# Kernel optimization log

Hardware: AMD Instinct MI355X
Metric: run time of the kernel (lower is better)

The kernel has to match this reference:

```python
import jax, jax.numpy as jnp
import numpy as np

HEADS = 8
BLOCK = 32

def setup_inputs() -> dict:
    key = jax.random.key(0)
    ks = jax.random.split(key, 4)
    b, n, d, f = 4, 4096, 1024, 128
    x = jax.random.normal(ks[0], (b, n, d), dtype=jnp.float32)
    w_qkv = jax.random.normal(ks[1], (3 * d, d), dtype=jnp.float32) * (d ** -0.5)
    w_out = jax.random.normal(ks[2], (d, d), dtype=jnp.float32) * (d ** -0.5)
    b_out = jnp.zeros((d,), dtype=jnp.float32)
    proj = jax.random.normal(ks[3], (HEADS, d // HEADS, f), dtype=jnp.float32) * ((d // HEADS) ** -0.5)
    return {"x": x, "w_qkv": w_qkv, "w_out": w_out, "b_out": b_out, "proj": proj}

def reference(x, w_qkv, w_out, b_out, proj):
    b, n, d = x.shape
    h = HEADS
    hd = d // h
    nb = n // BLOCK
    # QKV projection (torch Linear: x @ W.T)
    qkv = x @ w_qkv.T  # (b, n, 3d)
    q, k, v = jnp.split(qkv, 3, axis=-1)
    def to_blocks(t):
        # (b, n, d) -> (b, h, nb, BLOCK, hd)
        return t.reshape(b, n, h, hd).transpose(0, 2, 1, 3).reshape(b, h, nb, BLOCK, hd)
    q, k, v = to_blocks(q), to_blocks(k), to_blocks(v)
    # per-head feature map: elu(x @ proj) + 1
    qp = jax.nn.elu(jnp.einsum('bhcsd,hdf->bhcsf', q, proj)) + 1.0
    kp = jax.nn.elu(jnp.einsum('bhcsd,hdf->bhcsf', k, proj)) + 1.0
    # per-block kv state and normalizer
    kv = jnp.einsum('bhcsf,bhcsd->bhcfd', kp, v)          # (b,h,nb,f,hd)
    num = jnp.einsum('bhcsf,bhcfd->bhcsd', qp, kv)        # (b,h,nb,BLOCK,hd)
    ksum = kp.sum(axis=3)                                 # (b,h,nb,f)
    z = 1.0 / (jnp.einsum('bhcsf,bhcf->bhcs', qp, ksum) + 1e-8)
    out = num * z[..., None]
    # merge blocks and heads: (b,h,nb,BLOCK,hd) -> (b,n,d)
    out = out.reshape(b, h, n, hd).transpose(0, 2, 1, 3).reshape(b, n, d)
    # output projection (dropout inert in eval)
    return out @ w_out.T + b_out
```

## Files before the change

kernel.cpp:

```cpp
#include <hip/hip_runtime.h>
#include <hip/hip_bf16.h>
#include <stdint.h>
#include <stddef.h>

typedef __bf16 bf16_t;
typedef __bf16 bf16x8 __attribute__((ext_vector_type(8)));
typedef __bf16 bf16x4 __attribute__((ext_vector_type(4)));
typedef float  f32x4  __attribute__((ext_vector_type(4)));

static __device__ __forceinline__ f32x4 mfma16x16x32(bf16x8 a, bf16x8 b, f32x4 c) {
  return __builtin_amdgcn_mfma_f32_16x16x32_bf16(a, b, c, 0, 0, 0);
}

static __device__ __forceinline__ void gld_lds16(const void* g, void* l) {
  __builtin_amdgcn_global_load_lds(
      (const __attribute__((address_space(1))) unsigned int*)g,
      (__attribute__((address_space(3))) unsigned int*)l, 16, 0, 0);
}

#define BARW()   __builtin_amdgcn_s_barrier()
#define SCHED0() __builtin_amdgcn_sched_barrier(0)
#define LGKM0()  asm volatile("s_waitcnt lgkmcnt(0)" ::: "memory")
#define VMCNT(n) asm volatile("s_waitcnt vmcnt(" #n ")" ::: "memory")
#define PRIO(p)  __builtin_amdgcn_s_setprio(p)

__global__ __launch_bounds__(256) void prep(const float* __restrict__ wqkv,
                                            const float* __restrict__ proj,
                                            const float* __restrict__ wout,
                                            const float* __restrict__ x,
                                            bf16_t* __restrict__ B1t2,
                                            bf16_t* __restrict__ Wv,
                                            bf16_t* __restrict__ W3t,
                                            bf16_t* __restrict__ xbf) {
  const int b = blockIdx.x;
  const int tid = threadIdx.x;
  if (b >= 768) {
    for (int i = (b - 768) * 256 + tid; i < 4194304; i += 262144) {
      float4 v = *(const float4*)(x + (size_t)i * 4);
      bf16x4 o;
      o[0] = (bf16_t)v.x; o[1] = (bf16_t)v.y; o[2] = (bf16_t)v.z; o[3] = (bf16_t)v.w;
      *(bf16x4*)(xbf + (size_t)i * 4) = o;
    }
    return;
  }
  if (b >= 256) {
    const float* src = (b < 512) ? wout : (wqkv + (size_t)2048 * 1024);
    bf16_t* dst = (b < 512) ? W3t : Wv;
    size_t off = ((size_t)((b & 255)) * 4096) + tid * 16;
#pragma unroll
    for (int it = 0; it < 4; ++it) {
      float4 v = *(const float4*)(src + off + it * 4);
      bf16x4 o;
      o[0] = (bf16_t)v.x; o[1] = (bf16_t)v.y; o[2] = (bf16_t)v.z; o[3] = (bf16_t)v.w;
      *(bf16x4*)(dst + off + it * 4) = o;
    }
    return;
  }
  const int combo  = b >> 4;
  const int kt     = b & 15;
  const int qk     = combo >> 3;
  const int h      = combo & 7;
  const int klocal = tid & 63;
  const int fg     = tid >> 6;
  const int k      = kt * 64 + klocal;

  const float* wbase = wqkv + ((size_t)(qk * 1024 + h * 128)) * 1024 + k;
  const float* pbase = proj + (size_t)h * 16384 + fg * 32;

  float acc[32];
#pragma unroll
  for (int i = 0; i < 32; ++i) acc[i] = 0.f;

  for (int c = 0; c < 128; ++c) {
    float a = wbase[(size_t)c * 1024];
    const float4* p = (const float4*)(pbase + (size_t)c * 128);
#pragma unroll
    for (int i = 0; i < 8; ++i) {
      float4 pv = p[i];
      acc[i * 4 + 0] += a * pv.x;
      acc[i * 4 + 1] += a * pv.y;
      acc[i * 4 + 2] += a * pv.z;
      acc[i * 4 + 3] += a * pv.w;
    }
  }
  bf16_t* obase = B1t2 + ((size_t)(h * 256 + qk * 128 + fg * 32)) * 1024 + k;
#pragma unroll
  for (int i = 0; i < 32; ++i) obase[(size_t)i * 1024] = (bf16_t)acc[i];
}

#define GEMM_MAINLOOP_DECLS()                                                  \
  const int tid  = threadIdx.x;                                                \
  const int lane = tid & 63;                                                   \
  const int wid  = tid >> 6;                                                   \
  const int wm   = wid >> 2;                                                   \
  const int wn   = wid & 3;                                                    \
  const int lr   = lane & 15;                                                  \
  const int g0   = lane >> 4;                                                  \
  int srow[2], sgl[2];                                                         \
  _Pragma("unroll")                                                            \
  for (int l = 0; l < 2; ++l) {                                                \
    int idx = l * 512 + tid;                                                   \
    srow[l] = idx >> 3;                                                        \
    sgl[l]  = (idx & 7) ^ (srow[l] & 7);                                       \
  }

#define STAGE_T(arr, base, half, kt, K_)                                       \
  {                                                                            \
    const bf16_t* s_ = (base) + (size_t)((half) * 128) * (K_) + (kt) * 64;     \
    bf16_t* d_ = &(arr)[half][0];                                              \
    _Pragma("unroll")                                                          \
    for (int l_ = 0; l_ < 2; ++l_)                                             \
      gld_lds16(s_ + (size_t)srow[l_] * (K_) + sgl[l_] * 8,                    \
                d_ + (l_ * 512 + tid) * 8);                                    \
  }

#define RD_A(buf, qm)                                                          \
  _Pragma("unroll")                                                            \
  for (int t_ = 0; t_ < 4; ++t_) {                                             \
    int r_ = (qm) * 64 + t_ * 16 + lr;                                         \
    _Pragma("unroll")                                                          \
    for (int kh_ = 0; kh_ < 2; ++kh_) {                                        \
      int gl_ = (g0 + kh_ * 4) ^ (r_ & 7);                                     \
      a[t_][kh_] = *(const bf16x8*)(&sA[buf][wm][r_ * 64 + gl_ * 8]);          \
    }                                                                          \
  }
#define RD_B(buf, qn, breg)                                                    \
  _Pragma("unroll")                                                            \
  for (int u_ = 0; u_ < 2; ++u_) {                                             \
    int r_ = (wn & 1) * 64 + (qn) * 32 + u_ * 16 + lr;                         \
    _Pragma("unroll")                                                          \
    for (int kh_ = 0; kh_ < 2; ++kh_) {                                        \
      int gl_ = (g0 + kh_ * 4) ^ (r_ & 7);                                     \
      breg[u_][kh_] = *(const bf16x8*)(&sB[buf][wn >> 1][r_ * 64 + gl_ * 8]);  \
    }                                                                          \
  }
#define MMA(qm, qn, breg)                                                      \
  _Pragma("unroll")                                                            \
  for (int mi_ = 0; mi_ < 4; ++mi_)                                            \
    _Pragma("unroll")                                                          \
    for (int nj_ = 0; nj_ < 2; ++nj_)                                          \
      _Pragma("unroll")                                                        \
      for (int kh_ = 0; kh_ < 2; ++kh_)                                        \
        acc[(qm) * 4 + mi_][(qn) * 2 + nj_] =                                  \
            mfma16x16x32(a[mi_][kh_], breg[nj_][kh_],                          \
                         acc[(qm) * 4 + mi_][(qn) * 2 + nj_]);

#define GEMM_MAINLOOP_BODY(Abase, Bbase, K_, NT_)                              \
  f32x4 acc[8][4] = {};                                                        \
  bf16x8 a[4][2], b0[2][2], b1[2][2];                                          \
  STAGE_T(sB[0], Bbase, 0, 0, K_); STAGE_T(sA[0], Abase, 0, 0, K_);            \
  STAGE_T(sB[0], Bbase, 1, 0, K_); STAGE_T(sA[0], Abase, 1, 0, K_);            \
  STAGE_T(sB[1], Bbase, 0, 1, K_); STAGE_T(sA[1], Abase, 0, 1, K_);            \
  VMCNT(4);                                                                    \
  BARW();                                                                      \
  _Pragma("unroll 2")                                                          \
  for (int j = 0; j < (NT_); ++j) {                                            \
    const int cur = j & 1;                                                     \
    const int nxt = cur ^ 1;                                                   \
                       \
    RD_A(cur, 0);                                                              \
    RD_B(cur, 0, b0);                                                          \
    if (j + 1 < (NT_)) { STAGE_T(sB[nxt], Bbase, 1, j + 1, K_); }              \
    SCHED0(); BARW(); LGKM0(); SCHED0();                                       \
    PRIO(1); MMA(0, 0, b0); PRIO(0);                                           \
    SCHED0(); BARW();                                                          \
                             \
    RD_B(cur, 1, b1);                                                          \
    if (j + 1 < (NT_)) { STAGE_T(sA[nxt], Abase, 1, j + 1, K_); }              \
    SCHED0(); BARW(); LGKM0(); SCHED0();                                       \
    PRIO(1); MMA(0, 1, b1); PRIO(0);                                           \
    SCHED0(); BARW();                                                          \
                             \
    RD_A(cur, 1);                                                              \
    if (j + 2 < (NT_)) { STAGE_T(sB[cur], Bbase, 0, j + 2, K_); }              \
    SCHED0(); BARW(); LGKM0(); SCHED0();                                       \
    PRIO(1); MMA(1, 1, b1); PRIO(0);                                           \
    SCHED0(); BARW();                                                          \
                           \
    if (j + 2 < (NT_)) { STAGE_T(sA[cur], Abase, 0, j + 2, K_); }              \
    SCHED0(); BARW();                                                          \
    PRIO(1); MMA(1, 0, b0); PRIO(0);                                           \
    if (j + 2 < (NT_)) { VMCNT(4); } else { VMCNT(0); }                        \
    SCHED0(); BARW();                                                          \
  }

template <int EPI>
__global__ __launch_bounds__(512, 2) void gemm256(const bf16_t* __restrict__ A,
                                                  const bf16_t* __restrict__ Bt,
                                                  void* __restrict__ Cout,
                                                  const float* __restrict__ bias,
                                                  int N, int K, int NB) {
  __shared__ __align__(16) bf16_t sA[2][2][8192];
  __shared__ __align__(16) bf16_t sB[2][2][8192];
  GEMM_MAINLOOP_DECLS();

  const int nwg = gridDim.x;
  const int cpx = nwg >> 3;
  const int bid = blockIdx.x;
  const int swz = (bid & 7) * cpx + (bid >> 3);
  const int m0 = (swz / NB) * 256;
  const int n0 = (swz % NB) * 256;
  const int NT = K >> 6;

  const bf16_t* Abase = A  + (size_t)m0 * K;
  const bf16_t* Bbase = Bt + (size_t)n0 * K;

  GEMM_MAINLOOP_BODY(Abase, Bbase, K, NT);

#pragma unroll
  for (int i = 0; i < 8; ++i) {
#pragma unroll
    for (int jn = 0; jn < 4; ++jn) {
      const int n = n0 + wn * 64 + jn * 16 + lr;
#pragma unroll
      for (int r = 0; r < 4; ++r) {
        const int m = m0 + wm * 128 + i * 16 + g0 * 4 + r;
        float v = acc[i][jn][r];
        if constexpr (EPI == 2) {
          ((float*)Cout)[(size_t)m * N + n] = v + bias[n];
        } else {
          ((bf16_t*)Cout)[(size_t)m * N + n] = (bf16_t)v;
        }
      }
    }
  }
}

__global__ __launch_bounds__(512, 2) void gemm_fused(const bf16_t* __restrict__ A,
                                                     const bf16_t* __restrict__ Bt,
                                                     const bf16_t* __restrict__ VtG,
                                                     bf16_t* __restrict__ OUT1) {
  __shared__ __align__(16) bf16_t sA[2][2][8192];
  __shared__ __align__(16) bf16_t sB[2][2][8192];
  GEMM_MAINLOOP_DECLS();

  const int nwg = gridDim.x;
  const int cpx = nwg >> 3;
  const int bid = blockIdx.x;
  const int swz = (bid & 7) * cpx + (bid >> 3);
  const int m0 = (swz >> 3) * 256;
  const int h  = swz & 7;
  const int K  = 1024;
  const int NT = 16;

  const bf16_t* Abase = A  + (size_t)m0 * K;
  const bf16_t* Bbase = Bt + (size_t)(h * 256) * K;

  GEMM_MAINLOOP_BODY(Abase, Bbase, K, NT);

  char* sQb = (char*)(&sA[0][0][0]);
  char* sKb = (char*)(&sB[0][0][0]);

  {
    char* dbase = (wn < 2) ? sQb : sKb;
#pragma unroll
    for (int i = 0; i < 8; ++i)
#pragma unroll
      for (int jn = 0; jn < 4; ++jn)
#pragma unroll
        for (int r = 0; r < 4; ++r) {
          int row = wm * 128 + i * 16 + g0 * 4 + r;
          int col = (wn & 1) * 64 + jn * 16 + lr;
          float v = acc[i][jn][r];
          v = v > 0.f ? v + 1.f : __expf(v);
          int gq = col >> 3;
          int g  = (gq & 8) | ((gq ^ row) & 7);
          *(bf16_t*)(dbase + row * 256 + g * 16 + (col & 7) * 2) = (bf16_t)v;
        }
  }
  LGKM0();
  BARW();

  const int cb = wm * 4 + wn;
  const int rb = cb * 32;
  bf16x8 aS[4][2], bS[4][2];
#pragma unroll
  for (int kh = 0; kh < 4; ++kh) {
#pragma unroll
    for (int t = 0; t < 2; ++t) {
      int row = rb + t * 16 + lr;
      int gq = kh * 4 + g0;
      int g  = (gq & 8) | ((gq ^ row) & 7);
      aS[kh][t] = *(const bf16x8*)(sQb + row * 256 + g * 16);
      bS[kh][t] = *(const bf16x8*)(sKb + row * 256 + g * 16);
    }
  }
  SCHED0(); LGKM0(); BARW();

  {
#pragma unroll
    for (int l = 0; l < 8; ++l) {
      int gd = l * 512 + tid;
      int row = gd >> 5, gcol = gd & 31;
      const bf16_t* src = VtG + (size_t)(h * 128 + row) * 16384 + m0 +
                          ((gcol ^ (row & 7)) * 8);
      gld_lds16(src, sKb + gd * 16);
    }
  }
  SCHED0();

  f32x4 sacc[2][2] = {};
#pragma unroll
  for (int kh = 0; kh < 4; ++kh)
#pragma unroll
    for (int mt = 0; mt < 2; ++mt)
#pragma unroll
      for (int nt = 0; nt < 2; ++nt)
        sacc[mt][nt] = mfma16x16x32(aS[kh][mt], bS[kh][nt], sacc[mt][nt]);

  float zin[2][4];
#pragma unroll
  for (int mt = 0; mt < 2; ++mt)
#pragma unroll
    for (int r = 0; r < 4; ++r) {
      float s = sacc[mt][0][r] + sacc[mt][1][r];
      s += __shfl_xor(s, 1); s += __shfl_xor(s, 2);
      s += __shfl_xor(s, 4); s += __shfl_xor(s, 8);
      zin[mt][r] = 1.0f / (s + 1e-8f);
    }

  char* Pl = sQb;
#pragma unroll
  for (int mt = 0; mt < 2; ++mt)
#pragma unroll
    for (int nt = 0; nt < 2; ++nt)
#pragma unroll
      for (int r = 0; r < 4; ++r) {
        int i = mt * 16 + g0 * 4 + r;
        int jj = nt * 16 + lr;
        *(bf16_t*)(Pl + cb * 2560 + i * 80 + jj * 2) =
            (bf16_t)(sacc[mt][nt][r] * zin[mt][r]);
      }
  LGKM0();
  VMCNT(0);
  BARW();

  bf16x8 aP[2];
#pragma unroll
  for (int mt = 0; mt < 2; ++mt)
    aP[mt] = *(const bf16x8*)(Pl + cb * 2560 + (mt * 16 + lr) * 80 + g0 * 16);
#pragma unroll
  for (int dt = 0; dt < 8; ++dt) {
    int row = dt * 16 + lr;
    int gidx = cb * 4 + g0;
    int g = (gidx & 24) | ((gidx ^ row) & 7);
    bf16x8 bV = *(const bf16x8*)(sKb + row * 512 + g * 16);
#pragma unroll
    for (int mt = 0; mt < 2; ++mt) {
      f32x4 z = {};
      f32x4 o = mfma16x16x32(aP[mt], bV, z);
#pragma unroll
      for (int r = 0; r < 4; ++r) {
        int m = m0 + rb + mt * 16 + g0 * 4 + r;
        int d = h * 128 + dt * 16 + lr;
        OUT1[(size_t)m * 1024 + d] = (bf16_t)o[r];
      }
    }
  }
}

extern "C" void kernel_launch(void* const* d_in, const int* in_sizes, int n_in,
                              void* d_out, int out_size, void* d_ws, size_t ws_size,
                              hipStream_t stream) {
  const float* x     = (const float*)d_in[0];
  const float* w_qkv = (const float*)d_in[1];
  const float* w_out = (const float*)d_in[2];
  const float* b_out = (const float*)d_in[3];
  const float* proj  = (const float*)d_in[4];
  float* out = (float*)d_out;

  char* ws = (char*)d_ws;
  bf16_t* xbf  = (bf16_t*)(ws);
  bf16_t* B1t2 = (bf16_t*)(ws + 33554432);
  bf16_t* Wv   = (bf16_t*)(ws + 37748736);
  bf16_t* W3t  = (bf16_t*)(ws + 39845888);
  bf16_t* VtG  = (bf16_t*)(ws + 41943040);
  bf16_t* OUT1 = (bf16_t*)(ws + 75497472);

  (void)in_sizes; (void)n_in; (void)out_size; (void)ws_size;

  prep<<<1792, 256, 0, stream>>>(w_qkv, proj, w_out, x, B1t2, Wv, W3t, xbf);
  gemm256<3><<<256, 512, 0, stream>>>(Wv, xbf, (void*)VtG, nullptr, 16384, 1024, 64);
  gemm_fused<<<512, 512, 0, stream>>>(xbf, B1t2, VtG, OUT1);
  gemm256<2><<<256, 512, 0, stream>>>(OUT1, W3t, (void*)out, b_out, 1024, 1024, 4);
}
```

Before: 227.7 us.

## Load full tile fragments up front and cut GEMM mainloop barriers to two

The GEMM mainloop now reads all A and B fragments for the current k-tile into registers at the start of each iteration, using separate a0/a1 register sets. The four MMA quadrants then run back to back with global-to-LDS staging for tile j+2 placed between them, so only two barriers remain per iteration instead of eight. The prologue stages two full k-tiles and the wait count changes to match. This aims to cut synchronisation and LDS-wait stalls, at the cost of more live VGPRs, which could cause spills or lower occupancy under the 512x2 launch bound.

```diff
diff --git a/kernel.cpp b/kernel.cpp
--- a/kernel.cpp
+++ b/kernel.cpp
@@ -114,17 +114,17 @@
                 d_ + (l_ * 512 + tid) * 8);                                    \
   }
 
-#define RD_A(buf, qm)                                                          \
+#define RD_Aq(buf, qm, areg)                                                   \
   _Pragma("unroll")                                                            \
   for (int t_ = 0; t_ < 4; ++t_) {                                             \
     int r_ = (qm) * 64 + t_ * 16 + lr;                                         \
     _Pragma("unroll")                                                          \
     for (int kh_ = 0; kh_ < 2; ++kh_) {                                        \
       int gl_ = (g0 + kh_ * 4) ^ (r_ & 7);                                     \
-      a[t_][kh_] = *(const bf16x8*)(&sA[buf][wm][r_ * 64 + gl_ * 8]);          \
+      areg[t_][kh_] = *(const bf16x8*)(&sA[buf][wm][r_ * 64 + gl_ * 8]);       \
     }                                                                          \
   }
-#define RD_B(buf, qn, breg)                                                    \
+#define RD_Bq(buf, qn, breg)                                                   \
   _Pragma("unroll")                                                            \
   for (int u_ = 0; u_ < 2; ++u_) {                                             \
     int r_ = (wn & 1) * 64 + (qn) * 32 + u_ * 16 + lr;                         \
@@ -134,7 +134,7 @@
       breg[u_][kh_] = *(const bf16x8*)(&sB[buf][wn >> 1][r_ * 64 + gl_ * 8]);  \
     }                                                                          \
   }
-#define MMA(qm, qn, breg)                                                      \
+#define MMA(qm, qn, breg, areg)                                                \
   _Pragma("unroll")                                                            \
   for (int mi_ = 0; mi_ < 4; ++mi_)                                            \
     _Pragma("unroll")                                                          \
@@ -142,46 +142,39 @@
       _Pragma("unroll")                                                        \
       for (int kh_ = 0; kh_ < 2; ++kh_)                                        \
         acc[(qm) * 4 + mi_][(qn) * 2 + nj_] =                                  \
-            mfma16x16x32(a[mi_][kh_], breg[nj_][kh_],                          \
+            mfma16x16x32(areg[mi_][kh_], breg[nj_][kh_],                       \
                          acc[(qm) * 4 + mi_][(qn) * 2 + nj_]);
 
 #define GEMM_MAINLOOP_BODY(Abase, Bbase, K_, NT_)                              \
   f32x4 acc[8][4] = {};                                                        \
-  bf16x8 a[4][2], b0[2][2], b1[2][2];                                          \
-  STAGE_T(sB[0], Bbase, 0, 0, K_); STAGE_T(sA[0], Abase, 0, 0, K_);            \
-  STAGE_T(sB[0], Bbase, 1, 0, K_); STAGE_T(sA[0], Abase, 1, 0, K_);            \
-  STAGE_T(sB[1], Bbase, 0, 1, K_); STAGE_T(sA[1], Abase, 0, 1, K_);            \
-  VMCNT(4);                                                                    \
+  bf16x8 a0[4][2], a1[4][2], b0[2][2], b1[2][2];                               \
+  STAGE_T(sB[0], Bbase, 0, 0, K_); STAGE_T(sB[0], Bbase, 1, 0, K_);            \
+  STAGE_T(sA[0], Abase, 0, 0, K_); STAGE_T(sA[0], Abase, 1, 0, K_);            \
+  STAGE_T(sB[1], Bbase, 0, 1, K_); STAGE_T(sB[1], Bbase, 1, 1, K_);            \
+  STAGE_T(sA[1], Abase, 0, 1, K_); STAGE_T(sA[1], Abase, 1, 1, K_);            \
+  VMCNT(8);                                                                    \
   BARW();                                                                      \
   _Pragma("unroll 2")                                                          \
   for (int j = 0; j < (NT_); ++j) {                                            \
     const int cur = j & 1;                                                     \
-    const int nxt = cur ^ 1;                                                   \
-                       \
-    RD_A(cur, 0);                                                              \
-    RD_B(cur, 0, b0);                                                          \
-    if (j + 1 < (NT_)) { STAGE_T(sB[nxt], Bbase, 1, j + 1, K_); }              \
-    SCHED0(); BARW(); LGKM0(); SCHED0();                                       \
-    PRIO(1); MMA(0, 0, b0); PRIO(0);                                           \
-    SCHED0(); BARW();                                                          \
-                             \
-    RD_B(cur, 1, b1);                                                          \
-    if (j + 1 < (NT_)) { STAGE_T(sA[nxt], Abase, 1, j + 1, K_); }              \
-    SCHED0(); BARW(); LGKM0(); SCHED0();                                       \
-    PRIO(1); MMA(0, 1, b1); PRIO(0);                                           \
-    SCHED0(); BARW();                                                          \
-                             \
-    RD_A(cur, 1);                                                              \
+    RD_Aq(cur, 0, a0); RD_Aq(cur, 1, a1);                                      \
+    RD_Bq(cur, 0, b0); RD_Bq(cur, 1, b1);                                      \
+    SCHED0(); LGKM0(); SCHED0();                                               \
+    BARW(); SCHED0();                                                          \
+    PRIO(1); MMA(0, 0, b0, a0); PRIO(0); SCHED0();                             \
     if (j + 2 < (NT_)) { STAGE_T(sB[cur], Bbase, 0, j + 2, K_); }              \
-    SCHED0(); BARW(); LGKM0(); SCHED0();                                       \
-    PRIO(1); MMA(1, 1, b1); PRIO(0);                                           \
-    SCHED0(); BARW();                                                          \
-                           \
+    SCHED0();                                                                  \
+    PRIO(1); MMA(0, 1, b1, a0); PRIO(0); SCHED0();                             \
+    if (j + 2 < (NT_)) { STAGE_T(sB[cur], Bbase, 1, j + 2, K_); }              \
+    SCHED0();                                                                  \
+    PRIO(1); MMA(1, 1, b1, a1); PRIO(0); SCHED0();                             \
     if (j + 2 < (NT_)) { STAGE_T(sA[cur], Abase, 0, j + 2, K_); }              \
-    SCHED0(); BARW();                                                          \
-    PRIO(1); MMA(1, 0, b0); PRIO(0);                                           \
-    if (j + 2 < (NT_)) { VMCNT(4); } else { VMCNT(0); }                        \
-    SCHED0(); BARW();                                                          \
+    SCHED0();                                                                  \
+    PRIO(1); MMA(1, 0, b0, a1); PRIO(0); SCHED0();                             \
+    if (j + 2 < (NT_)) { STAGE_T(sA[cur], Abase, 1, j + 2, K_); VMCNT(8); }    \
+    else { VMCNT(0); }                                                         \
+    SCHED0();                                                                  \
+    BARW();                                                                    \
   }
 
 template <int EPI>
```

New measurement: 233.3 us. +2.5%, slower.
